# Kernel optimization log

Hardware: AMD Instinct MI355X
Metric: run time of the kernel (lower is better)

The kernel has to match this reference:

```python
import jax, jax.numpy as jnp
import numpy as np

OUTPUT_DIM = 2000
INPUT_DIM = 8192
N_COLS = 2000  # must equal OUTPUT_DIM so bias broadcasts over last dim as in the torch code
SPARSITY = 0.9
BLOCK = 4


def _apply_block_sparsity(weight, block=BLOCK, sparsity=SPARSITY, seed=1234):
    # Zero out 4x4 blocks with probability `sparsity`, mirroring apply_block_sparsity.
    rng = np.random.RandomState(seed)
    rb = (weight.shape[0] + block - 1) // block
    cb = (weight.shape[1] + block - 1) // block
    keep = (rng.rand(rb, cb) <= (1.0 - sparsity)).astype(np.float32)
    mask = np.kron(keep, np.ones((block, block), dtype=np.float32))
    return weight * mask[: weight.shape[0], : weight.shape[1]]


def setup_inputs() -> dict:
    key = jax.random.key(0)
    k_w, k_b, k_x = jax.random.split(key, 3)
    weight = np.asarray(jax.random.normal(k_w, (OUTPUT_DIM, INPUT_DIM), dtype=jnp.float32))
    weight = jnp.asarray(_apply_block_sparsity(weight))
    bias = jax.random.normal(k_b, (OUTPUT_DIM,), dtype=jnp.float32)
    x = jax.random.normal(k_x, (INPUT_DIM, N_COLS), dtype=jnp.float32)
    return {"weight": weight, "bias": bias, "x": x}


def reference(weight, bias, x):
    # [OUT, IN] @ [IN, N] -> [OUT, N]; bias [OUT] broadcasts over last dim (N == OUT here),
    # exactly matching torch.matmul(weight, x) + bias.
    return jnp.matmul(weight, x) + bias
```

## Files before the change

### kernel.cpp

```cpp
#include <hip/hip_runtime.h>

#define K_DIM 8192
#define M_REAL 2000
#define N_REAL 2000
#define M_PAD 2048
#define N_PAD 2048

#define BM 256
#define BN 256
#define BK 32
#define SPLITK 4
#define KSLAB (K_DIM / SPLITK)
#define NSTEP (KSLAB / BK)

#define NB_W 1024
#define NB_X 2048
#define NB_I 256

typedef __bf16 bf16x8 __attribute__((ext_vector_type(8)));
typedef float f32x4 __attribute__((ext_vector_type(4)));
typedef float fvec4 __attribute__((ext_vector_type(4)));

#define RAW_BARRIER()  asm volatile("s_barrier" ::: "memory")
#define LGKM0()        asm volatile("s_waitcnt lgkmcnt(0)" ::: "memory")
#define WAIT_VM8()     asm volatile("s_waitcnt vmcnt(8)" ::: "memory")
#define WAIT_VM4()     asm volatile("s_waitcnt vmcnt(4)" ::: "memory")
#define WAIT_VM0()     asm volatile("s_waitcnt vmcnt(0)" ::: "memory")

__device__ __forceinline__ unsigned short f2bf(float f) {
    union { float f; unsigned u; } v; v.f = f;
    unsigned r = v.u + 0x7FFFu + ((v.u >> 16) & 1u);
    return (unsigned short)(r >> 16);
}

__device__ __forceinline__ unsigned pk2(float a, float b) {
    return (unsigned)f2bf(a) | ((unsigned)f2bf(b) << 16);
}

__device__ __forceinline__ void async16(const void* g, void* l) {
    __builtin_amdgcn_global_load_lds((__attribute__((address_space(1))) void*)(g),
                                     (__attribute__((address_space(3))) void*)(l),
                                     16, 0, 0);
}

__global__ __launch_bounds__(256) void prep_kernel(const float* __restrict__ W,
                                                   const float* __restrict__ X,
                                                   const float* __restrict__ bias,
                                                   unsigned short* __restrict__ Wb,
                                                   unsigned short* __restrict__ XT,
                                                   float* __restrict__ out) {
    __shared__ unsigned short T[64][130];
    int bid = blockIdx.x;
    if (bid < NB_W) {
        unsigned tid = bid * 256u + threadIdx.x;
#pragma unroll
        for (unsigned i = 0; i < 8; ++i) {
            unsigned e = (i * (1024u * 256u) + tid) * 8u;
            uint4 o = make_uint4(0u, 0u, 0u, 0u);
            if (e < (unsigned)(M_REAL * K_DIM)) {
                fvec4 f0 = __builtin_nontemporal_load((const fvec4*)(W + e));
                fvec4 f1 = __builtin_nontemporal_load((const fvec4*)(W + e + 4));
                o.x = pk2(f0.x, f0.y);
                o.y = pk2(f0.z, f0.w);
                o.z = pk2(f1.x, f1.y);
                o.w = pk2(f1.z, f1.w);
            }
            *(uint4*)(Wb + e) = o;
        }
    } else if (bid < NB_W + NB_X) {
        int b = bid - NB_W;
        int k0 = (b & 63) << 7;
        int n0 = (b >> 6) << 6;
        int t = threadIdx.x;
        int c = t & 15;
        int r = t >> 4;
        int nl = c << 2;
        int n = n0 + nl;
        bool valid = (n < N_REAL);
#pragma unroll
        for (int p = 0; p < 4; ++p) {
            int kl = (r << 1) + (p << 5);
            fvec4 v0 = {0.f, 0.f, 0.f, 0.f};
            fvec4 v1 = {0.f, 0.f, 0.f, 0.f};
            if (valid) {
                v0 = __builtin_nontemporal_load((const fvec4*)(X + (k0 + kl) * N_REAL + n));
                v1 = __builtin_nontemporal_load((const fvec4*)(X + (k0 + kl + 1) * N_REAL + n));
            }
            *(unsigned*)&T[nl + 0][kl] = pk2(v0.x, v1.x);
            *(unsigned*)&T[nl + 1][kl] = pk2(v0.y, v1.y);
            *(unsigned*)&T[nl + 2][kl] = pk2(v0.z, v1.z);
            *(unsigned*)&T[nl + 3][kl] = pk2(v0.w, v1.w);
        }
        __syncthreads();
#pragma unroll
        for (int it = 0; it < 4; ++it) {
            int nl2 = r + (it << 4);
            int kl2 = c << 3;
            const unsigned* tp = (const unsigned*)&T[nl2][kl2];
            uint4 o;
            o.x = tp[0]; o.y = tp[1]; o.z = tp[2]; o.w = tp[3];
            *(uint4*)(XT + (((n0 + nl2) << 13) + k0 + kl2)) = o;
        }
    } else {
        const int total = M_REAL * (N_REAL / 4);
        for (int i = (bid - NB_W - NB_X) * 256 + (int)threadIdx.x; i < total; i += NB_I * 256) {
            int m = i / (N_REAL / 4);
            int n4 = i - m * (N_REAL / 4);
            float4 bv = *(const float4*)(bias + (n4 << 2));
            *(float4*)(out + m * N_REAL + (n4 << 2)) = bv;
        }
    }
}

__global__ __launch_bounds__(512, 2) void gemm_kernel(const unsigned short* __restrict__ Wb,
                                                      const unsigned short* __restrict__ XT,
                                                      float* __restrict__ out) {
    __shared__ __align__(16) unsigned short As[4][BM * BK];
    __shared__ __align__(16) unsigned short Bs[4][BN * BK];

    int f = blockIdx.x;
    int xcd = f & 7;
    int local = f >> 3;
    int bz = local & 3;
    int bx = (xcd & 3) * 2 + ((local >> 2) & 1);
    int by = (xcd >> 2) * 4 + (local >> 3);

    int t = threadIdx.x;
    int w = t >> 6;
    int l = t & 63;
    int wm = (w >> 2) * 128;
    int wn = (w & 3) * 64;
    int lane16 = l & 15;
    int quad = l >> 4;
    int m0 = by * BM;
    int n0 = bx * BN;
    int ks = bz * KSLAB;

    f32x4 acc[8][4] = {};

    int rlin = t >> 2;
    int ck = (t & 3) ^ (rlin & 3);
    const unsigned short* gA0 = Wb + (long long)(m0 + rlin) * K_DIM + ks + ck * 8;
    const unsigned short* gA1 = gA0 + 128LL * K_DIM;
    const unsigned short* gB0 = XT + (long long)(n0 + rlin) * K_DIM + ks + ck * 8;
    const unsigned short* gB1 = gB0 + 128LL * K_DIM;

    char* smA = (char*)&As[0][0];
    char* smB = (char*)&Bs[0][0];
    int wslot = w * 1024;

#define STAGE_A(OFF) do { \
        async16(gA0, smA + (OFF) + wslot); \
        async16(gA1, smA + (OFF) + 8192 + wslot); \
        gA0 += BK; gA1 += BK; } while (0)
#define STAGE_B(OFF) do { \
        async16(gB0, smB + (OFF) + wslot); \
        async16(gB1, smB + (OFF) + 8192 + wslot); \
        gB0 += BK; gB1 += BK; } while (0)

    int swz = ((quad ^ (lane16 & 3)) << 4);
    int arow = (wm + lane16) * 64 + swz;
    int brow = (wn + lane16) * 64 + swz;

    STAGE_A(0);     STAGE_B(0);
    STAGE_A(16384); STAGE_B(16384);
    STAGE_A(32768); STAGE_B(32768);
    WAIT_VM8();
    RAW_BARRIER();

    int cur = 0;
    int stg = 49152;

    bf16x8 a0, a1, a2, a3, b0, b1, b2, b3;

    for (int s = 0; s < NSTEP; ++s) {
        {
            const char* ab = smA + cur + arow;
            const char* bb = smB + cur + brow;
            a0 = *(const bf16x8*)(ab);
            a1 = *(const bf16x8*)(ab + 1024);
            a2 = *(const bf16x8*)(ab + 2048);
            a3 = *(const bf16x8*)(ab + 3072);
            b0 = *(const bf16x8*)(bb);
            b1 = *(const bf16x8*)(bb + 1024);
            b2 = *(const bf16x8*)(bb + 2048);
            b3 = *(const bf16x8*)(bb + 3072);
            if (s < NSTEP - 3) STAGE_A(stg);
            RAW_BARRIER();
            LGKM0();
            __builtin_amdgcn_s_setprio(1);
            acc[0][0] = __builtin_amdgcn_mfma_f32_16x16x32_bf16(a0, b0, acc[0][0], 0, 0, 0);
            acc[0][1] = __builtin_amdgcn_mfma_f32_16x16x32_bf16(a0, b1, acc[0][1], 0, 0, 0);
            acc[0][2] = __builtin_amdgcn_mfma_f32_16x16x32_bf16(a0, b2, acc[0][2], 0, 0, 0);
            acc[0][3] = __builtin_amdgcn_mfma_f32_16x16x32_bf16(a0, b3, acc[0][3], 0, 0, 0);
            acc[1][0] = __builtin_amdgcn_mfma_f32_16x16x32_bf16(a1, b0, acc[1][0], 0, 0, 0);
            acc[1][1] = __builtin_amdgcn_mfma_f32_16x16x32_bf16(a1, b1, acc[1][1], 0, 0, 0);
            acc[1][2] = __builtin_amdgcn_mfma_f32_16x16x32_bf16(a1, b2, acc[1][2], 0, 0, 0);
            acc[1][3] = __builtin_amdgcn_mfma_f32_16x16x32_bf16(a1, b3, acc[1][3], 0, 0, 0);
            acc[2][0] = __builtin_amdgcn_mfma_f32_16x16x32_bf16(a2, b0, acc[2][0], 0, 0, 0);
            acc[2][1] = __builtin_amdgcn_mfma_f32_16x16x32_bf16(a2, b1, acc[2][1], 0, 0, 0);
            acc[2][2] = __builtin_amdgcn_mfma_f32_16x16x32_bf16(a2, b2, acc[2][2], 0, 0, 0);
            acc[2][3] = __builtin_amdgcn_mfma_f32_16x16x32_bf16(a2, b3, acc[2][3], 0, 0, 0);
            acc[3][0] = __builtin_amdgcn_mfma_f32_16x16x32_bf16(a3, b0, acc[3][0], 0, 0, 0);
            acc[3][1] = __builtin_amdgcn_mfma_f32_16x16x32_bf16(a3, b1, acc[3][1], 0, 0, 0);
            acc[3][2] = __builtin_amdgcn_mfma_f32_16x16x32_bf16(a3, b2, acc[3][2], 0, 0, 0);
            acc[3][3] = __builtin_amdgcn_mfma_f32_16x16x32_bf16(a3, b3, acc[3][3], 0, 0, 0);
            __builtin_amdgcn_s_setprio(0);
            RAW_BARRIER();
        }
        {
            const char* ab = smA + cur + arow + 4096;
            a0 = *(const bf16x8*)(ab);
            a1 = *(const bf16x8*)(ab + 1024);
            a2 = *(const bf16x8*)(ab + 2048);
            a3 = *(const bf16x8*)(ab + 3072);
            if (s < NSTEP - 3) {
                STAGE_B(stg);
                WAIT_VM8();
            } else if (s == NSTEP - 3) {
                WAIT_VM4();
            } else if (s == NSTEP - 2) {
                WAIT_VM0();
            }
            RAW_BARRIER();
            LGKM0();
            __builtin_amdgcn_s_setprio(1);
            acc[4][0] = __builtin_amdgcn_mfma_f32_16x16x32_bf16(a0, b0, acc[4][0], 0, 0, 0);
            acc[4][1] = __builtin_amdgcn_mfma_f32_16x16x32_bf16(a0, b1, acc[4][1], 0, 0, 0);
            acc[4][2] = __builtin_amdgcn_mfma_f32_16x16x32_bf16(a0, b2, acc[4][2], 0, 0, 0);
            acc[4][3] = __builtin_amdgcn_mfma_f32_16x16x32_bf16(a0, b3, acc[4][3], 0, 0, 0);
            acc[5][0] = __builtin_amdgcn_mfma_f32_16x16x32_bf16(a1, b0, acc[5][0], 0, 0, 0);
            acc[5][1] = __builtin_amdgcn_mfma_f32_16x16x32_bf16(a1, b1, acc[5][1], 0, 0, 0);
            acc[5][2] = __builtin_amdgcn_mfma_f32_16x16x32_bf16(a1, b2, acc[5][2], 0, 0, 0);
            acc[5][3] = __builtin_amdgcn_mfma_f32_16x16x32_bf16(a1, b3, acc[5][3], 0, 0, 0);
            acc[6][0] = __builtin_amdgcn_mfma_f32_16x16x32_bf16(a2, b0, acc[6][0], 0, 0, 0);
            acc[6][1] = __builtin_amdgcn_mfma_f32_16x16x32_bf16(a2, b1, acc[6][1], 0, 0, 0);
            acc[6][2] = __builtin_amdgcn_mfma_f32_16x16x32_bf16(a2, b2, acc[6][2], 0, 0, 0);
            acc[6][3] = __builtin_amdgcn_mfma_f32_16x16x32_bf16(a2, b3, acc[6][3], 0, 0, 0);
            acc[7][0] = __builtin_amdgcn_mfma_f32_16x16x32_bf16(a3, b0, acc[7][0], 0, 0, 0);
            acc[7][1] = __builtin_amdgcn_mfma_f32_16x16x32_bf16(a3, b1, acc[7][1], 0, 0, 0);
            acc[7][2] = __builtin_amdgcn_mfma_f32_16x16x32_bf16(a3, b2, acc[7][2], 0, 0, 0);
            acc[7][3] = __builtin_amdgcn_mfma_f32_16x16x32_bf16(a3, b3, acc[7][3], 0, 0, 0);
            __builtin_amdgcn_s_setprio(0);
            RAW_BARRIER();
        }
        cur = (cur + 16384) & 65535;
        stg = (stg + 16384) & 65535;
    }
#undef STAGE_A
#undef STAGE_B

#pragma unroll
    for (int j = 0; j < 4; ++j) {
        int n = n0 + wn + j * 16 + lane16;
        if (n >= N_REAL) continue;
#pragma unroll
        for (int i = 0; i < 8; ++i) {
            int mbase = m0 + wm + i * 16 + quad * 4;
#pragma unroll
            for (int r = 0; r < 4; ++r) {
                int m = mbase + r;
                if (m < M_REAL)
                    atomicAdd(&out[(long long)m * N_REAL + n], acc[i][j][r]);
            }
        }
    }
}

extern "C" void kernel_launch(void* const* d_in, const int* in_sizes, int n_in,
                              void* d_out, int out_size, void* d_ws, size_t ws_size,
                              hipStream_t stream) {
    const float* W    = (const float*)d_in[0];
    const float* bias = (const float*)d_in[1];
    const float* X    = (const float*)d_in[2];
    float* out = (float*)d_out;

    unsigned short* Wb = (unsigned short*)d_ws;
    unsigned short* XT = Wb + (long long)M_PAD * K_DIM;

    prep_kernel<<<NB_W + NB_X + NB_I, 256, 0, stream>>>(W, X, bias, Wb, XT, out);

    gemm_kernel<<<(N_PAD / BN) * (M_PAD / BM) * SPLITK, 512, 0, stream>>>(Wb, XT, out);
}
```

Baseline: 260.3 us.

## Fuse fp32-to-bf16 conversion and transpose into GEMM register-staged pipeline

Removes the separate prep pass that converted W and X to bf16 workspace buffers. The GEMM now loads fp32 tiles of W and X straight into registers, converts them to bf16 and writes them transposed and swizzled into LDS with a double buffer. This drops the extra global read, write and re-read of the converted operands. In exchange each block reads twice the bytes per tile, loses the async global-to-LDS path, uses more registers for staging, and fetches X with strided row loads.

Measured after the change: 285.1 us. 1.1x slower.

```diff
diff --git a/kernel.cpp b/kernel.cpp
--- a/kernel.cpp
+++ b/kernel.cpp
@@ -13,110 +13,31 @@
 #define KSLAB (K_DIM / SPLITK)
 #define NSTEP (KSLAB / BK)
 
-#define NB_W 1024
-#define NB_X 2048
-#define NB_I 256
-
 typedef __bf16 bf16x8 __attribute__((ext_vector_type(8)));
+typedef __bf16 bf16x4 __attribute__((ext_vector_type(4)));
 typedef float f32x4 __attribute__((ext_vector_type(4)));
 typedef float fvec4 __attribute__((ext_vector_type(4)));
 
 #define RAW_BARRIER()  asm volatile("s_barrier" ::: "memory")
 #define LGKM0()        asm volatile("s_waitcnt lgkmcnt(0)" ::: "memory")
-#define WAIT_VM8()     asm volatile("s_waitcnt vmcnt(8)" ::: "memory")
-#define WAIT_VM4()     asm volatile("s_waitcnt vmcnt(4)" ::: "memory")
-#define WAIT_VM0()     asm volatile("s_waitcnt vmcnt(0)" ::: "memory")
-
-__device__ __forceinline__ unsigned short f2bf(float f) {
-    union { float f; unsigned u; } v; v.f = f;
-    unsigned r = v.u + 0x7FFFu + ((v.u >> 16) & 1u);
-    return (unsigned short)(r >> 16);
-}
-
-__device__ __forceinline__ unsigned pk2(float a, float b) {
-    return (unsigned)f2bf(a) | ((unsigned)f2bf(b) << 16);
-}
-
-__device__ __forceinline__ void async16(const void* g, void* l) {
-    __builtin_amdgcn_global_load_lds((__attribute__((address_space(1))) void*)(g),
-                                     (__attribute__((address_space(3))) void*)(l),
-                                     16, 0, 0);
-}
-
-__global__ __launch_bounds__(256) void prep_kernel(const float* __restrict__ W,
-                                                   const float* __restrict__ X,
-                                                   const float* __restrict__ bias,
-                                                   unsigned short* __restrict__ Wb,
-                                                   unsigned short* __restrict__ XT,
-                                                   float* __restrict__ out) {
-    __shared__ unsigned short T[64][130];
-    int bid = blockIdx.x;
-    if (bid < NB_W) {
-        unsigned tid = bid * 256u + threadIdx.x;
-#pragma unroll
-        for (unsigned i = 0; i < 8; ++i) {
-            unsigned e = (i * (1024u * 256u) + tid) * 8u;
-            uint4 o = make_uint4(0u, 0u, 0u, 0u);
-            if (e < (unsigned)(M_REAL * K_DIM)) {
-                fvec4 f0 = __builtin_nontemporal_load((const fvec4*)(W + e));
-                fvec4 f1 = __builtin_nontemporal_load((const fvec4*)(W + e + 4));
-                o.x = pk2(f0.x, f0.y);
-                o.y = pk2(f0.z, f0.w);
-                o.z = pk2(f1.x, f1.y);
-                o.w = pk2(f1.z, f1.w);
-            }
-            *(uint4*)(Wb + e) = o;
-        }
-    } else if (bid < NB_W + NB_X) {
-        int b = bid - NB_W;
-        int k0 = (b & 63) << 7;
-        int n0 = (b >> 6) << 6;
-        int t = threadIdx.x;
-        int c = t & 15;
-        int r = t >> 4;
-        int nl = c << 2;
-        int n = n0 + nl;
-        bool valid = (n < N_REAL);
-#pragma unroll
-        for (int p = 0; p < 4; ++p) {
-            int kl = (r << 1) + (p << 5);
-            fvec4 v0 = {0.f, 0.f, 0.f, 0.f};
-            fvec4 v1 = {0.f, 0.f, 0.f, 0.f};
-            if (valid) {
-                v0 = __builtin_nontemporal_load((const fvec4*)(X + (k0 + kl) * N_REAL + n));
-                v1 = __builtin_nontemporal_load((const fvec4*)(X + (k0 + kl + 1) * N_REAL + n));
-            }
-            *(unsigned*)&T[nl + 0][kl] = pk2(v0.x, v1.x);
-            *(unsigned*)&T[nl + 1][kl] = pk2(v0.y, v1.y);
-            *(unsigned*)&T[nl + 2][kl] = pk2(v0.z, v1.z);
-            *(unsigned*)&T[nl + 3][kl] = pk2(v0.w, v1.w);
-        }
-        __syncthreads();
-#pragma unroll
-        for (int it = 0; it < 4; ++it) {
-            int nl2 = r + (it << 4);
-            int kl2 = c << 3;
-            const unsigned* tp = (const unsigned*)&T[nl2][kl2];
-            uint4 o;
-            o.x = tp[0]; o.y = tp[1]; o.z = tp[2]; o.w = tp[3];
-            *(uint4*)(XT + (((n0 + nl2) << 13) + k0 + kl2)) = o;
-        }
-    } else {
-        const int total = M_REAL * (N_REAL / 4);
-        for (int i = (bid - NB_W - NB_X) * 256 + (int)threadIdx.x; i < total; i += NB_I * 256) {
-            int m = i / (N_REAL / 4);
-            int n4 = i - m * (N_REAL / 4);
-            float4 bv = *(const float4*)(bias + (n4 << 2));
-            *(float4*)(out + m * N_REAL + (n4 << 2)) = bv;
-        }
+
+__device__ __forceinline__ __bf16 tobf(float f) { return (__bf16)f; }
+
+__global__ __launch_bounds__(256) void prep_init(const float* __restrict__ bias,
+                                                 float* __restrict__ out) {
+    const int total = M_REAL * (N_REAL / 4);
+    for (int i = blockIdx.x * 256 + threadIdx.x; i < total; i += 1024 * 256) {
+        int m = i / (N_REAL / 4);
+        int n4 = i - m * (N_REAL / 4);
+        float4 bv = *(const float4*)(bias + (n4 << 2));
+        *(float4*)(out + m * N_REAL + (n4 << 2)) = bv;
     }
 }
 
-__global__ __launch_bounds__(512, 2) void gemm_kernel(const unsigned short* __restrict__ Wb,
-                                                      const unsigned short* __restrict__ XT,
+__global__ __launch_bounds__(512, 2) void gemm_kernel(const float* __restrict__ W,
+                                                      const float* __restrict__ X,
                                                       float* __restrict__ out) {
-    __shared__ __align__(16) unsigned short As[4][BM * BK];
-    __shared__ __align__(16) unsigned short Bs[4][BN * BK];
+    __shared__ __align__(16) char sm[65536];
 
     int f = blockIdx.x;
     int xcd = f & 7;
@@ -138,117 +59,144 @@
 
     f32x4 acc[8][4] = {};
 
-    int rlin = t >> 2;
-    int ck = (t & 3) ^ (rlin & 3);
-    const unsigned short* gA0 = Wb + (long long)(m0 + rlin) * K_DIM + ks + ck * 8;
-    const unsigned short* gA1 = gA0 + 128LL * K_DIM;
-    const unsigned short* gB0 = XT + (long long)(n0 + rlin) * K_DIM + ks + ck * 8;
-    const unsigned short* gB1 = gB0 + 128LL * K_DIM;
-
-    char* smA = (char*)&As[0][0];
-    char* smB = (char*)&Bs[0][0];
-    int wslot = w * 1024;
-
-#define STAGE_A(OFF) do { \
-        async16(gA0, smA + (OFF) + wslot); \
-        async16(gA1, smA + (OFF) + 8192 + wslot); \
-        gA0 += BK; gA1 += BK; } while (0)
-#define STAGE_B(OFF) do { \
-        async16(gB0, smB + (OFF) + wslot); \
-        async16(gB1, smB + (OFF) + 8192 + wslot); \
-        gB0 += BK; gB1 += BK; } while (0)
+    int mA   = t >> 1;
+    int khA  = (t & 1) * 16;
+    int rowA = m0 + mA;
+    bool aValid = (rowA < M_REAL);
+    int rowAc = aValid ? rowA : 0;
+    int a_c0 = (((t & 1) * 2) ^ (mA & 3)) << 4;
+    char* daBase = sm + mA * 64;
+
+    int kg  = t >> 6;
+    int nb  = (t & 63) * 4;
+    int nB  = n0 + nb;
+    bool bValid = (nB < N_REAL);
+    int nBc = bValid ? nB : 0;
+    int cB  = kg >> 1;
+    int h8  = (kg & 1) * 8;
+    int b_o0 = ((cB ^ 0) << 4) + h8;
+    int b_o1 = ((cB ^ 1) << 4) + h8;
+    int b_o2 = ((cB ^ 2) << 4) + h8;
+    int b_o3 = ((cB ^ 3) << 4) + h8;
+    char* dbBase = sm + 32768 + nb * 64;
+    long long kgOff = (long long)(kg * 4) * N_REAL;
+
+    fvec4 wa0, wa1, wa2, wa3, xb0, xb1, xb2, xb3;
+    const fvec4 z4 = {0.f, 0.f, 0.f, 0.f};
+
+#define LOADG(KB) do { \
+        const float* pa = W + (long long)rowAc * K_DIM + (KB) + khA; \
+        wa0 = *(const fvec4*)(pa); \
+        wa1 = *(const fvec4*)(pa + 4); \
+        wa2 = *(const fvec4*)(pa + 8); \
+        wa3 = *(const fvec4*)(pa + 12); \
+        if (!aValid) { wa0 = z4; wa1 = z4; wa2 = z4; wa3 = z4; } \
+        const float* pb = X + (long long)(KB) * N_REAL + kgOff + nBc; \
+        xb0 = *(const fvec4*)(pb); \
+        xb1 = *(const fvec4*)(pb + N_REAL); \
+        xb2 = *(const fvec4*)(pb + 2 * N_REAL); \
+        xb3 = *(const fvec4*)(pb + 3 * N_REAL); \
+        if (!bValid) { xb0 = z4; xb1 = z4; xb2 = z4; xb3 = z4; } \
+    } while (0)
+
+#define WRITET(BUFO) do { \
+        bf16x8 h0, h1; \
+        h0[0] = tobf(wa0[0]); h0[1] = tobf(wa0[1]); h0[2] = tobf(wa0[2]); h0[3] = tobf(wa0[3]); \
+        h0[4] = tobf(wa1[0]); h0[5] = tobf(wa1[1]); h0[6] = tobf(wa1[2]); h0[7] = tobf(wa1[3]); \
+        h1[0] = tobf(wa2[0]); h1[1] = tobf(wa2[1]); h1[2] = tobf(wa2[2]); h1[3] = tobf(wa2[3]); \
+        h1[4] = tobf(wa3[0]); h1[5] = tobf(wa3[1]); h1[6] = tobf(wa3[2]); h1[7] = tobf(wa3[3]); \
+        *(bf16x8*)(daBase + (BUFO) + a_c0) = h0; \
+        *(bf16x8*)(daBase + (BUFO) + (a_c0 ^ 16)) = h1; \
+        bf16x4 v0, v1, v2, v3; \
+        v0[0] = tobf(xb0[0]); v0[1] = tobf(xb1[0]); v0[2] = tobf(xb2[0]); v0[3] = tobf(xb3[0]); \
+        v1[0] = tobf(xb0[1]); v1[1] = tobf(xb1[1]); v1[2] = tobf(xb2[1]); v1[3] = tobf(xb3[1]); \
+        v2[0] = tobf(xb0[2]); v2[1] = tobf(xb1[2]); v2[2] = tobf(xb2[2]); v2[3] = tobf(xb3[2]); \
+        v3[0] = tobf(xb0[3]); v3[1] = tobf(xb1[3]); v3[2] = tobf(xb2[3]); v3[3] = tobf(xb3[3]); \
+        *(bf16x4*)(dbBase + (BUFO) + b_o0) = v0; \
+        *(bf16x4*)(dbBase + (BUFO) + 64 + b_o1) = v1; \
+        *(bf16x4*)(dbBase + (BUFO) + 128 + b_o2) = v2; \
+        *(bf16x4*)(dbBase + (BUFO) + 192 + b_o3) = v3; \
+    } while (0)
 
     int swz = ((quad ^ (lane16 & 3)) << 4);
     int arow = (wm + lane16) * 64 + swz;
     int brow = (wn + lane16) * 64 + swz;
 
-    STAGE_A(0);     STAGE_B(0);
-    STAGE_A(16384); STAGE_B(16384);
-    STAGE_A(32768); STAGE_B(32768);
-    WAIT_VM8();
+    LOADG(ks);
+    WRITET(0);
+    LOADG(ks + BK);
+    LGKM0();
     RAW_BARRIER();
 
-    int cur = 0;
-    int stg = 49152;
-
     bf16x8 a0, a1, a2, a3, b0, b1, b2, b3;
 
     for (int s = 0; s < NSTEP; ++s) {
-        {
-            const char* ab = smA + cur + arow;
-            const char* bb = smB + cur + brow;
-            a0 = *(const bf16x8*)(ab);
-            a1 = *(const bf16x8*)(ab + 1024);
-            a2 = *(const bf16x8*)(ab + 2048);
-            a3 = *(const bf16x8*)(ab + 3072);
-            b0 = *(const bf16x8*)(bb);
-            b1 = *(const bf16x8*)(bb + 1024);
-            b2 = *(const bf16x8*)(bb + 2048);
-            b3 = *(const bf16x8*)(bb + 3072);
-            if (s < NSTEP - 3) STAGE_A(stg);
-            RAW_BARRIER();
-            LGKM0();
-            __builtin_amdgcn_s_setprio(1);
-            acc[0][0] = __builtin_amdgcn_mfma_f32_16x16x32_bf16(a0, b0, acc[0][0], 0, 0, 0);
-            acc[0][1] = __builtin_amdgcn_mfma_f32_16x16x32_bf16(a0, b1, acc[0][1], 0, 0, 0);
-            acc[0][2] = __builtin_amdgcn_mfma_f32_16x16x32_bf16(a0, b2, acc[0][2], 0, 0, 0);
-            acc[0][3] = __builtin_amdgcn_mfma_f32_16x16x32_bf16(a0, b3, acc[0][3], 0, 0, 0);
-            acc[1][0] = __builtin_amdgcn_mfma_f32_16x16x32_bf16(a1, b0, acc[1][0], 0, 0, 0);
-            acc[1][1] = __builtin_amdgcn_mfma_f32_16x16x32_bf16(a1, b1, acc[1][1], 0, 0, 0);
-            acc[1][2] = __builtin_amdgcn_mfma_f32_16x16x32_bf16(a1, b2, acc[1][2], 0, 0, 0);
-            acc[1][3] = __builtin_amdgcn_mfma_f32_16x16x32_bf16(a1, b3, acc[1][3], 0, 0, 0);
-            acc[2][0] = __builtin_amdgcn_mfma_f32_16x16x32_bf16(a2, b0, acc[2][0], 0, 0, 0);
-            acc[2][1] = __builtin_amdgcn_mfma_f32_16x16x32_bf16(a2, b1, acc[2][1], 0, 0, 0);
-            acc[2][2] = __builtin_amdgcn_mfma_f32_16x16x32_bf16(a2, b2, acc[2][2], 0, 0, 0);
-            acc[2][3] = __builtin_amdgcn_mfma_f32_16x16x32_bf16(a2, b3, acc[2][3], 0, 0, 0);
-            acc[3][0] = __builtin_amdgcn_mfma_f32_16x16x32_bf16(a3, b0, acc[3][0], 0, 0, 0);
-            acc[3][1] = __builtin_amdgcn_mfma_f32_16x16x32_bf16(a3, b1, acc[3][1], 0, 0, 0);
-            acc[3][2] = __builtin_amdgcn_mfma_f32_16x16x32_bf16(a3, b2, acc[3][2], 0, 0, 0);
-            acc[3][3] = __builtin_amdgcn_mfma_f32_16x16x32_bf16(a3, b3, acc[3][3], 0, 0, 0);
-            __builtin_amdgcn_s_setprio(0);
-            RAW_BARRIER();
+        int curo = (s & 1) << 14;
+        const char* Ab = sm + curo + arow;
+        const char* Bb = sm + 32768 + curo + brow;
+        a0 = *(const bf16x8*)(Ab);
+        a1 = *(const bf16x8*)(Ab + 1024);
+        a2 = *(const bf16x8*)(Ab + 2048);
+        a3 = *(const bf16x8*)(Ab + 3072);
+        b0 = *(const bf16x8*)(Bb);
+        b1 = *(const bf16x8*)(Bb + 1024);
+        b2 = *(const bf16x8*)(Bb + 2048);
+        b3 = *(const bf16x8*)(Bb + 3072);
+
+        if (s + 1 < NSTEP) {
+            WRITET(curo ^ 16384);
+            if (s + 2 < NSTEP)
+                LOADG(ks + (s + 2) * BK);
         }
-        {
-            const char* ab = smA + cur + arow + 4096;
-            a0 = *(const bf16x8*)(ab);
-            a1 = *(const bf16x8*)(ab + 1024);
-            a2 = *(const bf16x8*)(ab + 2048);
-            a3 = *(const bf16x8*)(ab + 3072);
-            if (s < NSTEP - 3) {
-                STAGE_B(stg);
-                WAIT_VM8();
-            } else if (s == NSTEP - 3) {
-                WAIT_VM4();
-            } else if (s == NSTEP - 2) {
-                WAIT_VM0();
-            }
-            RAW_BARRIER();
-            LGKM0();
-            __builtin_amdgcn_s_setprio(1);
-            acc[4][0] = __builtin_amdgcn_mfma_f32_16x16x32_bf16(a0, b0, acc[4][0], 0, 0, 0);
-            acc[4][1] = __builtin_amdgcn_mfma_f32_16x16x32_bf16(a0, b1, acc[4][1], 0, 0, 0);
-            acc[4][2] = __builtin_amdgcn_mfma_f32_16x16x32_bf16(a0, b2, acc[4][2], 0, 0, 0);
-            acc[4][3] = __builtin_amdgcn_mfma_f32_16x16x32_bf16(a0, b3, acc[4][3], 0, 0, 0);
-            acc[5][0] = __builtin_amdgcn_mfma_f32_16x16x32_bf16(a1, b0, acc[5][0], 0, 0, 0);
-            acc[5][1] = __builtin_amdgcn_mfma_f32_16x16x32_bf16(a1, b1, acc[5][1], 0, 0, 0);
-            acc[5][2] = __builtin_amdgcn_mfma_f32_16x16x32_bf16(a1, b2, acc[5][2], 0, 0, 0);
-            acc[5][3] = __builtin_amdgcn_mfma_f32_16x16x32_bf16(a1, b3, acc[5][3], 0, 0, 0);
-            acc[6][0] = __builtin_amdgcn_mfma_f32_16x16x32_bf16(a2, b0, acc[6][0], 0, 0, 0);
-            acc[6][1] = __builtin_amdgcn_mfma_f32_16x16x32_bf16(a2, b1, acc[6][1], 0, 0, 0);
-            acc[6][2] = __builtin_amdgcn_mfma_f32_16x16x32_bf16(a2, b2, acc[6][2], 0, 0, 0);
-            acc[6][3] = __builtin_amdgcn_mfma_f32_16x16x32_bf16(a2, b3, acc[6][3], 0, 0, 0);
-            acc[7][0] = __builtin_amdgcn_mfma_f32_16x16x32_bf16(a3, b0, acc[7][0], 0, 0, 0);
-            acc[7][1] = __builtin_amdgcn_mfma_f32_16x16x32_bf16(a3, b1, acc[7][1], 0, 0, 0);
-            acc[7][2] = __builtin_amdgcn_mfma_f32_16x16x32_bf16(a3, b2, acc[7][2], 0, 0, 0);
-            acc[7][3] = __builtin_amdgcn_mfma_f32_16x16x32_bf16(a3, b3, acc[7][3], 0, 0, 0);
-            __builtin_amdgcn_s_setprio(0);
-            RAW_BARRIER();
-        }
-        cur = (cur + 16384) & 65535;
-        stg = (stg + 16384) & 65535;
+
+        __builtin_amdgcn_s_setprio(1);
+        acc[0][0] = __builtin_amdgcn_mfma_f32_16x16x32_bf16(a0, b0, acc[0][0], 0, 0, 0);
+        acc[0][1] = __builtin_amdgcn_mfma_f32_16x16x32_bf16(a0, b1, acc[0][1], 0, 0, 0);
+        acc[0][2] = __builtin_amdgcn_mfma_f32_16x16x32_bf16(a0, b2, acc[0][2], 0, 0, 0);
+        acc[0][3] = __builtin_amdgcn_mfma_f32_16x16x32_bf16(a0, b3, acc[0][3], 0, 0, 0);
+        acc[1][0] = __builtin_amdgcn_mfma_f32_16x16x32_bf16(a1, b0, acc[1][0], 0, 0, 0);
+        acc[1][1] = __builtin_amdgcn_mfma_f32_16x16x32_bf16(a1, b1, acc[1][1], 0, 0, 0);
+        acc[1][2] = __builtin_amdgcn_mfma_f32_16x16x32_bf16(a1, b2, acc[1][2], 0, 0, 0);
+        acc[1][3] = __builtin_amdgcn_mfma_f32_16x16x32_bf16(a1, b3, acc[1][3], 0, 0, 0);
+        acc[2][0] = __builtin_amdgcn_mfma_f32_16x16x32_bf16(a2, b0, acc[2][0], 0, 0, 0);
+        acc[2][1] = __builtin_amdgcn_mfma_f32_16x16x32_bf16(a2, b1, acc[2][1], 0, 0, 0);
+        acc[2][2] = __builtin_amdgcn_mfma_f32_16x16x32_bf16(a2, b2, acc[2][2], 0, 0, 0);
+        acc[2][3] = __builtin_amdgcn_mfma_f32_16x16x32_bf16(a2, b3, acc[2][3], 0, 0, 0);
+        acc[3][0] = __builtin_amdgcn_mfma_f32_16x16x32_bf16(a3, b0, acc[3][0], 0, 0, 0);
+        acc[3][1] = __builtin_amdgcn_mfma_f32_16x16x32_bf16(a3, b1, acc[3][1], 0, 0, 0);
+        acc[3][2] = __builtin_amdgcn_mfma_f32_16x16x32_bf16(a3, b2, acc[3][2], 0, 0, 0);
+        acc[3][3] = __builtin_amdgcn_mfma_f32_16x16x32_bf16(a3, b3, acc[3][3], 0, 0, 0);
+        __builtin_amdgcn_s_setprio(0);
+
+        a0 = *(const bf16x8*)(Ab + 4096);
+        a1 = *(const bf16x8*)(Ab + 5120);
+        a2 = *(const bf16x8*)(Ab + 6144);
+        a3 = *(const bf16x8*)(Ab + 7168);
+
+        LGKM0();
+        RAW_BARRIER();
+
+        __builtin_amdgcn_s_setprio(1);
+        acc[4][0] = __builtin_amdgcn_mfma_f32_16x16x32_bf16(a0, b0, acc[4][0], 0, 0, 0);
+        acc[4][1] = __builtin_amdgcn_mfma_f32_16x16x32_bf16(a0, b1, acc[4][1], 0, 0, 0);
+        acc[4][2] = __builtin_amdgcn_mfma_f32_16x16x32_bf16(a0, b2, acc[4][2], 0, 0, 0);
+        acc[4][3] = __builtin_amdgcn_mfma_f32_16x16x32_bf16(a0, b3, acc[4][3], 0, 0, 0);
+        acc[5][0] = __builtin_amdgcn_mfma_f32_16x16x32_bf16(a1, b0, acc[5][0], 0, 0, 0);
+        acc[5][1] = __builtin_amdgcn_mfma_f32_16x16x32_bf16(a1, b1, acc[5][1], 0, 0, 0);
+        acc[5][2] = __builtin_amdgcn_mfma_f32_16x16x32_bf16(a1, b2, acc[5][2], 0, 0, 0);
+        acc[5][3] = __builtin_amdgcn_mfma_f32_16x16x32_bf16(a1, b3, acc[5][3], 0, 0, 0);
+        acc[6][0] = __builtin_amdgcn_mfma_f32_16x16x32_bf16(a2, b0, acc[6][0], 0, 0, 0);
+        acc[6][1] = __builtin_amdgcn_mfma_f32_16x16x32_bf16(a2, b1, acc[6][1], 0, 0, 0);
+        acc[6][2] = __builtin_amdgcn_mfma_f32_16x16x32_bf16(a2, b2, acc[6][2], 0, 0, 0);
+        acc[6][3] = __builtin_amdgcn_mfma_f32_16x16x32_bf16(a2, b3, acc[6][3], 0, 0, 0);
+        acc[7][0] = __builtin_amdgcn_mfma_f32_16x16x32_bf16(a3, b0, acc[7][0], 0, 0, 0);
+        acc[7][1] = __builtin_amdgcn_mfma_f32_16x16x32_bf16(a3, b1, acc[7][1], 0, 0, 0);
+        acc[7][2] = __builtin_amdgcn_mfma_f32_16x16x32_bf16(a3, b2, acc[7][2], 0, 0, 0);
+        acc[7][3] = __builtin_amdgcn_mfma_f32_16x16x32_bf16(a3, b3, acc[7][3], 0, 0, 0);
+        __builtin_amdgcn_s_setprio(0);
     }
-#undef STAGE_A
-#undef STAGE_B
+#undef LOADG
+#undef WRITET
 
 #pragma unroll
     for (int j = 0; j < 4; ++j) {
@@ -274,11 +222,8 @@
     const float* bias = (const float*)d_in[1];
     const float* X    = (const float*)d_in[2];
     float* out = (float*)d_out;
-
-    unsigned short* Wb = (unsigned short*)d_ws;
-    unsigned short* XT = Wb + (long long)M_PAD * K_DIM;
-
-    prep_kernel<<<NB_W + NB_X + NB_I, 256, 0, stream>>>(W, X, bias, Wb, XT, out);
-
-    gemm_kernel<<<(N_PAD / BN) * (M_PAD / BM) * SPLITK, 512, 0, stream>>>(Wb, XT, out);
+    (void)d_ws; (void)ws_size;
+
+    prep_init<<<1024, 256, 0, stream>>>(bias, out);
+    gemm_kernel<<<(N_PAD / BN) * (M_PAD / BM) * SPLITK, 512, 0, stream>>>(W, X, out);
 }
```
